# Performance work log

Measured on AMD Instinct MI355X. Metric: run time of the kernel, lower is better.

## Reference

```python
import jax, jax.numpy as jnp
import numpy as np

D_MODEL = 768
N_HEADS = 12
D_HEAD = D_MODEL // N_HEADS
TEMP = float(np.sqrt(D_HEAD))


def setup_inputs() -> dict:
    key = jax.random.key(0)
    ks = jax.random.split(key, 12)
    B, S, D = 8, 2048, D_MODEL
    patches = jax.random.normal(ks[0], (B, S, D), dtype=jnp.float32)
    in_weight = jax.random.uniform(ks[1], (D * 3, D), dtype=jnp.float32)
    in_bias = jax.random.uniform(ks[2], (D * 3,), dtype=jnp.float32)
    out_w = jax.random.normal(ks[3], (D, D), dtype=jnp.float32) * (1.0 / np.sqrt(D))
    out_b = jnp.zeros((D,), dtype=jnp.float32)
    mlp_w1 = jax.random.normal(ks[4], (4 * D, D), dtype=jnp.float32) * (1.0 / np.sqrt(D))
    mlp_b1 = jnp.zeros((4 * D,), dtype=jnp.float32)
    mlp_w2 = jax.random.normal(ks[5], (D, 4 * D), dtype=jnp.float32) * (1.0 / np.sqrt(4 * D))
    mlp_b2 = jnp.zeros((D,), dtype=jnp.float32)
    ln1_g = jnp.ones((D,), dtype=jnp.float32)
    ln1_b = jnp.zeros((D,), dtype=jnp.float32)
    ln2_g = jnp.ones((D,), dtype=jnp.float32)
    ln2_b = jnp.zeros((D,), dtype=jnp.float32)
    return {
        "patches": patches,
        "in_weight": in_weight, "in_bias": in_bias,
        "out_w": out_w, "out_b": out_b,
        "mlp_w1": mlp_w1, "mlp_b1": mlp_b1,
        "mlp_w2": mlp_w2, "mlp_b2": mlp_b2,
        "ln1_g": ln1_g, "ln1_b": ln1_b,
        "ln2_g": ln2_g, "ln2_b": ln2_b,
    }


def layer_norm(x, g, b, eps=1e-5):
    mu = jnp.mean(x, axis=-1, keepdims=True)
    var = jnp.var(x, axis=-1, keepdims=True)
    return (x - mu) * jax.lax.rsqrt(var + eps) * g + b


def mha(x, in_weight, in_bias, out_w, out_b):
    # Replicate quirky per-head reshape: [3D, D] -> [H, d_head, 3, D]
    W = in_weight.reshape(N_HEADS, D_HEAD, 3, D_MODEL)  # h, e, 3, d
    Bv = in_bias.reshape(N_HEADS, D_HEAD, 3)            # h, e, 3
    qw, kw, vw = W[:, :, 0, :], W[:, :, 1, :], W[:, :, 2, :]  # [H, e, D]
    qb, kb, vb = Bv[:, :, 0], Bv[:, :, 1], Bv[:, :, 2]        # [H, e]
    # Q,K,V per head: [B, H, S, e]
    Q = jnp.einsum('bsd,hed->bhse', x, qw) + qb[None, :, None, :]
    K = jnp.einsum('bsd,hed->bhse', x, kw) + kb[None, :, None, :]
    V = jnp.einsum('bsd,hed->bhse', x, vw) + vb[None, :, None, :]
    atn = jnp.einsum('bhse,bhte->bhst', Q, K)
    atn = jax.nn.softmax(atn / TEMP, axis=-1)
    # NOTE: original uses V (not atn @ V) as head output; heads concatenated over feature dim
    B_, H, S, e = V.shape
    heads = jnp.transpose(V, (0, 2, 1, 3)).reshape(B_, S, H * e)
    masks = jnp.sum(atn, axis=1)  # sum over heads: [B, S, S]
    out = heads @ out_w.T + out_b
    return out, masks


def reference(patches, in_weight, in_bias, out_w, out_b,
              mlp_w1, mlp_b1, mlp_w2, mlp_b2,
              ln1_g, ln1_b, ln2_g, ln2_b):
    x = layer_norm(patches, ln1_g, ln1_b)
    sa, _ = mha(x, in_weight, in_bias, out_w, out_b)
    x = sa + x  # dropout = identity (eval)
    x = layer_norm(x, ln2_g, ln2_b)
    h = jax.nn.selu(x @ mlp_w1.T + mlp_b1)
    x = (h @ mlp_w2.T + mlp_b2) + x
    return x
```

## Files before the change

kernel.cpp:

```cpp
#include <hip/hip_runtime.h>


typedef __bf16 bf16;
typedef __bf16 bf16x8 __attribute__((ext_vector_type(8)));
typedef __bf16 bf16x4 __attribute__((ext_vector_type(4)));
typedef float  f32x4  __attribute__((ext_vector_type(4)));

#define N_ROWS  16384

#define AS1(p) ((const __attribute__((address_space(1))) void*)(p))
#define AS3(p) ((__attribute__((address_space(3))) void*)(p))

#define WAIT8  __builtin_amdgcn_s_waitcnt(0x0F78)
#define WAIT6  __builtin_amdgcn_s_waitcnt(0x0F76)
#define WAIT2  __builtin_amdgcn_s_waitcnt(0x0F72)
#define WAIT0  __builtin_amdgcn_s_waitcnt(0x0F70)
#define NOWAIT (void)0

#define N1 589824
#define N2 589824
#define N3 147456
__global__ __launch_bounds__(256) void prep_cast(const float* __restrict__ w1,
                                                 const float* __restrict__ w2,
                                                 const float* __restrict__ ow,
                                                 bf16* __restrict__ w1b,
                                                 bf16* __restrict__ w2b,
                                                 bf16* __restrict__ owb) {
  int i = blockIdx.x * 256 + threadIdx.x;
  const float* src; bf16* dst; int off;
  if (i < N1)           { src = w1; dst = w1b; off = i; }
  else if (i < N1 + N2) { src = w2; dst = w2b; off = i - N1; }
  else                  { src = ow; dst = owb; off = i - N1 - N2; }
  float4 v = ((const float4*)src)[off];
  bf16x4 o = {(bf16)v.x, (bf16)v.y, (bf16)v.z, (bf16)v.w};
  *(bf16x4*)(dst + 4 * (size_t)off) = o;
}

__global__ __launch_bounds__(256) void wvt_kernel(const float* __restrict__ in_weight,
                                                  bf16* __restrict__ wvt) {
  __shared__ float t[64][65];
  const int k0 = blockIdx.x * 64, j0 = blockIdx.y * 64;
  const int tx = threadIdx.x & 63, ty = threadIdx.x >> 6;
  for (int jj = ty; jj < 64; jj += 4)
    t[jj][tx] = in_weight[((size_t)(j0 + jj) * 3 + 2) * 768 + k0 + tx];
  __syncthreads();
  for (int kk = ty; kk < 64; kk += 4)
    wvt[(size_t)(k0 + kk) * 768 + j0 + tx] = (bf16)t[tx][kk];
}

__global__ __launch_bounds__(64) void bias_combine_kernel(const float* __restrict__ out_w,
                                                          const float* __restrict__ in_bias,
                                                          const float* __restrict__ out_b,
                                                          float* __restrict__ bc) {
  int n = blockIdx.x, l = threadIdx.x;
  float s = 0.f;
  for (int j = l; j < 768; j += 64) s += out_w[(size_t)n * 768 + j] * in_bias[j * 3 + 2];
#pragma unroll
  for (int off = 32; off > 0; off >>= 1) s += __shfl_xor(s, off, 64);
  if (l == 0) bc[n] = s + out_b[n];
}

template <typename TIN>
__global__ __launch_bounds__(256) void ln_kernel(const TIN* __restrict__ x,
                                                 const float* __restrict__ g,
                                                 const float* __restrict__ b,
                                                 bf16* __restrict__ y) {
  const int row = blockIdx.x;
  const TIN* xr = x + (size_t)row * 768;
  float v[3], s1 = 0.f, s2 = 0.f;
#pragma unroll
  for (int i = 0; i < 3; ++i) {
    v[i] = (float)xr[threadIdx.x + i * 256];
    s1 += v[i];
    s2 += v[i] * v[i];
  }
#pragma unroll
  for (int off = 32; off > 0; off >>= 1) {
    s1 += __shfl_xor(s1, off, 64);
    s2 += __shfl_xor(s2, off, 64);
  }
  __shared__ float red[8];
  int w = threadIdx.x >> 6, l = threadIdx.x & 63;
  if (l == 0) { red[w * 2] = s1; red[w * 2 + 1] = s2; }
  __syncthreads();
  s1 = red[0] + red[2] + red[4] + red[6];
  s2 = red[1] + red[3] + red[5] + red[7];
  const float mu = s1 * (1.f / 768.f);
  const float var = s2 * (1.f / 768.f) - mu * mu;
  const float rstd = rsqrtf(var + 1e-5f);
#pragma unroll
  for (int i = 0; i < 3; ++i) {
    int d = threadIdx.x + i * 256;
    y[(size_t)row * 768 + d] = (bf16)((v[i] - mu) * rstd * g[d] + b[d]);
  }
}

template <int EPI>
__global__ __launch_bounds__(512, 2) void gemm_bt(const bf16* __restrict__ A,
                                                  const bf16* __restrict__ B,
                                                  const float* __restrict__ bias,
                                                  const bf16* __restrict__ resid,
                                                  void* __restrict__ out,
                                                  int M, int N, int K) {
  __shared__ bf16 ring[65536];
  const int tid = threadIdx.x;
  const int w = tid >> 6, l = tid & 63;
  const int wr = w >> 2, wcn = w & 3;
  const int q = l >> 4, m16 = l & 15;

  int mtile, ntile;
  {
    const int L = blockIdx.y * gridDim.x + blockIdx.x;
    const int gy = gridDim.y;
    if ((gy & 7) == 0) {
      const int mpx = gy >> 3;
      const int xcd = L & 7;
      const int slot = L >> 3;
      mtile = xcd * mpx + (slot % mpx);
      ntile = slot / mpx;
    } else {
      mtile = blockIdx.y; ntile = blockIdx.x;
    }
  }
  const long tileM = (long)mtile * 256;
  const long tileN = (long)ntile * 256;

  const bf16* gA[2][2]; const bf16* gB[2][2];
  int lA[2][2], lB[2][2];
  {
    const int sc = l & 3;
#pragma unroll
    for (int j = 0; j < 2; ++j) {
      const int b = w * 2 + j;
      const int p = b >> 3, s = (b >> 2) & 1, blk = b & 3;
#pragma unroll
      for (int mh = 0; mh < 2; ++mh) {
        const int row = s * 128 + mh * 64 + blk * 16 + (l >> 2);
        const int cl = (sc - (row >> 1)) & 3;
        gA[mh][j] = A + (tileM + row) * (long)K + p * 32 + cl * 8;
        lA[mh][j] = p * 8192 + row * 32 + sc * 8;
      }
      const int rowB = b * 16 + (l >> 2);
      const int clB = (sc - (rowB >> 1)) & 3;
#pragma unroll
      for (int ks = 0; ks < 2; ++ks) {
        gB[ks][j] = B + (tileN + rowB) * (long)K + ks * 32 + clB * 8;
        lB[ks][j] = 16384 + ks * 8192 + rowB * 32 + sc * 8;
      }
    }
  }

  int offA[8], offB[4];
#pragma unroll
  for (int mh = 0; mh < 2; ++mh)
#pragma unroll
    for (int mi = 0; mi < 4; ++mi) {
      const int r = wr * 128 + mh * 64 + mi * 16 + m16;
      offA[mh * 4 + mi] = r * 32 + (((q + (r >> 1)) & 3) << 3);
    }
#pragma unroll
  for (int ni = 0; ni < 4; ++ni) {
    const int r = wcn * 64 + ni * 16 + m16;
    offB[ni] = r * 32 + (((q + (r >> 1)) & 3) << 3);
  }

  f32x4 acc[8][4] = {};

  int kb0A0 = 0, kb0B0 = 0, kb0B1 = 0, kb0A1 = 0;
  int kb1A0 = 64, kb1B0 = 64, kb1B1 = 64, kb1A1 = 64;

#define ST(BP, LO, BUF, KV)                                                    \
  { bf16* bb = ring + (BUF) * 32768;                                           \
    __builtin_amdgcn_global_load_lds(AS1((BP)[0] + (KV)), AS3(bb + (LO)[0]), 16, 0, 0); \
    __builtin_amdgcn_global_load_lds(AS1((BP)[1] + (KV)), AS3(bb + (LO)[1]), 16, 0, 0); \
    (KV) += 128; }

  ST(gA[0], lA[0], 0, kb0A0) ST(gB[0], lB[0], 0, kb0B0)
  ST(gA[1], lA[1], 0, kb0A1) ST(gB[1], lB[1], 0, kb0B1)
  ST(gB[1], lB[1], 1, kb1B1) ST(gA[1], lA[1], 1, kb1A1)
  WAIT6;
  __builtin_amdgcn_s_barrier();

  bf16x8 bv[4];
#define PHASE(BUF, MH, KS, LB, STG, WSTMT)                                     \
  {                                                                            \
    const bf16* pa = ring + (BUF) * 32768 + (KS) * 8192;                       \
    const bf16* pb = ring + (BUF) * 32768 + 16384 + (KS) * 8192;               \
    bf16x8 af[4];                                                              \
    _Pragma("unroll")                                                          \
    for (int mi = 0; mi < 4; ++mi)                                             \
      af[mi] = *(const bf16x8*)&pa[offA[(MH) * 4 + mi]];                       \
    if (LB) {                                                                  \
      _Pragma("unroll")                                                        \
      for (int ni = 0; ni < 4; ++ni)                                           \
        bv[ni] = *(const bf16x8*)&pb[offB[ni]];                                \
    }                                                                          \
    STG;                                                                       \
    WSTMT;                                                                     \
    __builtin_amdgcn_s_barrier();                                              \
    asm volatile("s_waitcnt lgkmcnt(0)");                                      \
    __builtin_amdgcn_s_setprio(1);                                             \
    _Pragma("unroll")                                                          \
    for (int mi = 0; mi < 4; ++mi) {                                           \
      _Pragma("unroll")                                                        \
      for (int ni = 0; ni < 4; ++ni)                                           \
        acc[(MH) * 4 + mi][ni] = __builtin_amdgcn_mfma_f32_16x16x32_bf16(      \
            af[mi], bv[ni], acc[(MH) * 4 + mi][ni], 0, 0, 0);                  \
    }                                                                          \
    __builtin_amdgcn_s_setprio(0);                                             \
    __builtin_amdgcn_s_barrier();                                              \
  }

  const int T = K >> 6;
#pragma unroll 1
  for (int i = 0; i < T / 2 - 1; ++i) {
    PHASE(0, 0, 0, 1, ST(gA[0], lA[0], 1, kb1A0), NOWAIT)
    PHASE(0, 1, 0, 0, ST(gB[0], lB[0], 1, kb1B0), WAIT8)
    PHASE(0, 1, 1, 1, ST(gB[0], lB[0], 0, kb0B0), NOWAIT)
    PHASE(0, 0, 1, 0, ST(gA[1], lA[1], 0, kb0A1), WAIT6)
    PHASE(1, 0, 1, 1, ST(gA[0], lA[0], 0, kb0A0), NOWAIT)
    PHASE(1, 1, 1, 0, ST(gB[1], lB[1], 0, kb0B1), WAIT8)
    PHASE(1, 1, 0, 1, ST(gB[1], lB[1], 1, kb1B1), NOWAIT)
    PHASE(1, 0, 0, 0, ST(gA[1], lA[1], 1, kb1A1), WAIT6)
  }
  PHASE(0, 0, 0, 1, ST(gA[0], lA[0], 1, kb1A0), NOWAIT)
  PHASE(0, 1, 0, 0, ST(gB[0], lB[0], 1, kb1B0), WAIT8)
  PHASE(0, 1, 1, 1, (void)0, NOWAIT)
  PHASE(0, 0, 1, 0, (void)0, WAIT2)
  PHASE(1, 0, 1, 1, (void)0, NOWAIT)
  PHASE(1, 1, 1, 0, (void)0, WAIT0)
  PHASE(1, 1, 0, 1, (void)0, NOWAIT)
  PHASE(1, 0, 0, 0, (void)0, NOWAIT)
#undef PHASE
#undef ST

  const long colBase = tileN + (long)wcn * 64 + m16;
  const long rowBase = tileM + (long)wr * 128 + q * 4;
#pragma unroll
  for (int mi = 0; mi < 8; ++mi) {
#pragma unroll
    for (int r = 0; r < 4; ++r) {
      const long row = rowBase + mi * 16 + r;
#pragma unroll
      for (int ni = 0; ni < 4; ++ni) {
        const long col = colBase + ni * 16;
        float v = acc[mi][ni][r];
        if (EPI == 0) {
          ((bf16*)out)[row * N + col] = (bf16)v;
        } else if (EPI == 1) {
          v += bias[col] + (float)resid[row * N + col];
          ((float*)out)[row * N + col] = v;
        } else if (EPI == 2) {
          v += bias[col];
          v = v > 0.f ? 1.0507009873554805f * v
                      : 1.0507009873554805f * 1.6732632423543772f * (__expf(v) - 1.f);
          ((bf16*)out)[row * N + col] = (bf16)v;
        } else {
          v += bias[col] + (float)resid[row * N + col];
          ((bf16*)out)[row * N + col] = (bf16)v;
        }
      }
    }
  }
}

extern "C" void kernel_launch(void* const* d_in, const int* in_sizes, int n_in,
                              void* d_out, int out_size, void* d_ws, size_t ws_size,
                              hipStream_t stream) {
  const float* patches   = (const float*)d_in[0];
  const float* in_weight = (const float*)d_in[1];
  const float* in_bias   = (const float*)d_in[2];
  const float* out_w     = (const float*)d_in[3];
  const float* out_b     = (const float*)d_in[4];
  const float* mlp_w1    = (const float*)d_in[5];
  const float* mlp_b1    = (const float*)d_in[6];
  const float* mlp_w2    = (const float*)d_in[7];
  const float* mlp_b2    = (const float*)d_in[8];
  const float* ln1_g     = (const float*)d_in[9];
  const float* ln1_b     = (const float*)d_in[10];
  const float* ln2_g     = (const float*)d_in[11];
  const float* ln2_b     = (const float*)d_in[12];

  char* ws = (char*)d_ws;
  const size_t MB = 1024 * 1024;
  bf16* Wc   = (bf16*)(ws + 0);
  bf16* w1b  = (bf16*)(ws + 2 * MB);
  bf16* w2b  = (bf16*)(ws + 8 * MB);
  bf16* owb  = (bf16*)(ws + 14 * MB);
  bf16* wvt  = (bf16*)(ws + 16 * MB);
  float* bc  = (float*)(ws + 18 * MB);
  bf16* X1   = (bf16*)(ws + 20 * MB);
  bf16* X3   = (bf16*)(ws + 20 * MB);
  bf16* X2b  = (bf16*)(ws + 48 * MB);
  bf16* H    = (bf16*)(ws + 48 * MB);

  prep_cast<<<(N1 + N2 + N3) / 256, 256, 0, stream>>>(mlp_w1, mlp_w2, out_w,
                                                      w1b, w2b, owb);
  wvt_kernel<<<dim3(12, 12), 256, 0, stream>>>(in_weight, wvt);
  bias_combine_kernel<<<768, 64, 0, stream>>>(out_w, in_bias, out_b, bc);
  gemm_bt<0><<<dim3(3, 3), 512, 0, stream>>>(owb, wvt, nullptr, nullptr, Wc, 768, 768, 768);

  ln_kernel<float><<<N_ROWS, 256, 0, stream>>>(patches, ln1_g, ln1_b, X1);
  gemm_bt<3><<<dim3(3, 64), 512, 0, stream>>>(X1, Wc, bc, X1, X2b, N_ROWS, 768, 768);
  ln_kernel<bf16><<<N_ROWS, 256, 0, stream>>>(X2b, ln2_g, ln2_b, X3);
  gemm_bt<2><<<dim3(12, 64), 512, 0, stream>>>(X3, w1b, mlp_b1, nullptr, H, N_ROWS, 3072, 768);
  gemm_bt<1><<<dim3(3, 64), 512, 0, stream>>>(H, w2b, mlp_b2, X3, d_out, N_ROWS, 768, 3072);
}
```

Baseline: 390.1 us.

## Add 128x128-tile GEMM kernel with 3-stage LDS ring for MLP GEMMs

```diff
diff --git a/kernel.cpp b/kernel.cpp
--- a/kernel.cpp
+++ b/kernel.cpp
@@ -11,6 +11,8 @@
 #define AS1(p) ((const __attribute__((address_space(1))) void*)(p))
 #define AS3(p) ((__attribute__((address_space(3))) void*)(p))
 
+#define VM4 0x0F74
+#define VM0 0x0F70
 #define WAIT8  __builtin_amdgcn_s_waitcnt(0x0F78)
 #define WAIT6  __builtin_amdgcn_s_waitcnt(0x0F76)
 #define WAIT2  __builtin_amdgcn_s_waitcnt(0x0F72)
@@ -95,8 +97,145 @@
   }
 }
 
+#define SLOT_E (256 * 32)
 template <int EPI>
-__global__ __launch_bounds__(512, 2) void gemm_bt(const bf16* __restrict__ A,
+__global__ __launch_bounds__(256, 3) void gemm128(const bf16* __restrict__ A,
+                                                  const bf16* __restrict__ B,
+                                                  const float* __restrict__ bias,
+                                                  const bf16* __restrict__ resid,
+                                                  void* __restrict__ out,
+                                                  int M, int N, int K) {
+  __shared__ bf16 ring[3 * SLOT_E];
+  const int tid = threadIdx.x;
+  const int w = tid >> 6, l = tid & 63;
+  const int wr = w >> 1, wcn = w & 1;
+  const int q = l >> 4, m16 = l & 15;
+
+  int mtile, ntile;
+  {
+    const int L = blockIdx.y * gridDim.x + blockIdx.x;
+    const int gy = gridDim.y;
+    if ((gy & 7) == 0) {
+      const int mpx = gy >> 3;
+      const int xcd = L & 7;
+      const int slot = L >> 3;
+      mtile = xcd * mpx + (slot % mpx);
+      ntile = slot / mpx;
+    } else {
+      mtile = blockIdx.y; ntile = blockIdx.x;
+    }
+  }
+  const long tileM = (long)mtile * 128;
+  const long tileN = (long)ntile * 128;
+
+  const bf16* gA[2]; int ldA[2];
+  const bf16* gB[2]; int ldB[2];
+#pragma unroll
+  for (int j = 0; j < 2; ++j) {
+    const int ch = tid + j * 256;
+    const int row = ch >> 2;
+    const int cl = ((ch & 3) - (row >> 1)) & 3;
+    gA[j] = A + (tileM + row) * (long)K + cl * 8;
+    gB[j] = B + (tileN + row) * (long)K + cl * 8;
+    ldA[j] = ch * 8;
+    ldB[j] = ch * 8;
+  }
+
+  int offA[4], offB[4];
+#pragma unroll
+  for (int mi = 0; mi < 4; ++mi) {
+    const int r = wr * 64 + mi * 16 + m16;
+    offA[mi] = r * 32 + (((q + (r >> 1)) & 3) << 3);
+  }
+#pragma unroll
+  for (int ni = 0; ni < 4; ++ni) {
+    const int r = wcn * 64 + ni * 16 + m16;
+    offB[ni] = r * 32 + (((q + (r >> 1)) & 3) << 3);
+  }
+
+  f32x4 acc[4][4] = {};
+
+#pragma unroll
+  for (int s = 0; s < 2; ++s) {
+    bf16* da = ring + s * SLOT_E;
+    bf16* db = da + 128 * 32;
+#pragma unroll
+    for (int j = 0; j < 2; ++j) {
+      __builtin_amdgcn_global_load_lds(AS1(gA[j] + s * 32), AS3(&da[ldA[j]]), 16, 0, 0);
+      __builtin_amdgcn_global_load_lds(AS1(gB[j] + s * 32), AS3(&db[ldB[j]]), 16, 0, 0);
+    }
+  }
+  long k_next = 64;
+
+#define KSTEP(SLOT, WIMM, ISSUE)                                               \
+  {                                                                            \
+    __builtin_amdgcn_s_waitcnt(WIMM);                                          \
+    __builtin_amdgcn_s_barrier();                                              \
+    if (ISSUE) {                                                               \
+      bf16* da = ring + (((SLOT) + 2) % 3) * SLOT_E;                           \
+      bf16* db = da + 128 * 32;                                                \
+      _Pragma("unroll")                                                        \
+      for (int j = 0; j < 2; ++j) {                                            \
+        __builtin_amdgcn_global_load_lds(AS1(gA[j] + k_next), AS3(&da[ldA[j]]), 16, 0, 0); \
+        __builtin_amdgcn_global_load_lds(AS1(gB[j] + k_next), AS3(&db[ldB[j]]), 16, 0, 0); \
+      }                                                                        \
+      k_next += 32;                                                            \
+    }                                                                          \
+    const bf16* ca = ring + (SLOT) * SLOT_E;                                   \
+    const bf16* cb = ca + 128 * 32;                                            \
+    bf16x8 bfr[4];                                                             \
+    _Pragma("unroll")                                                          \
+    for (int ni = 0; ni < 4; ++ni) bfr[ni] = *(const bf16x8*)&cb[offB[ni]];    \
+    _Pragma("unroll")                                                          \
+    for (int mi = 0; mi < 4; ++mi) {                                           \
+      const bf16x8 af = *(const bf16x8*)&ca[offA[mi]];                         \
+      _Pragma("unroll")                                                        \
+      for (int ni = 0; ni < 4; ++ni)                                           \
+        acc[mi][ni] = __builtin_amdgcn_mfma_f32_16x16x32_bf16(af, bfr[ni],     \
+                                                              acc[mi][ni], 0, 0, 0); \
+    }                                                                          \
+  }
+
+  const int T = K >> 5;
+#pragma unroll 1
+  for (int g = 0; g < T - 3; g += 3) {
+    KSTEP(0, VM4, 1) KSTEP(1, VM4, 1) KSTEP(2, VM4, 1)
+  }
+  KSTEP(0, VM4, 1) KSTEP(1, VM4, 0) KSTEP(2, VM0, 0)
+#undef KSTEP
+
+  const long colBase = tileN + (long)wcn * 64 + m16;
+  const long rowBase = tileM + (long)wr * 64 + q * 4;
+#pragma unroll
+  for (int mi = 0; mi < 4; ++mi) {
+#pragma unroll
+    for (int r = 0; r < 4; ++r) {
+      const long row = rowBase + mi * 16 + r;
+#pragma unroll
+      for (int ni = 0; ni < 4; ++ni) {
+        const long col = colBase + ni * 16;
+        float v = acc[mi][ni][r];
+        if (EPI == 0) {
+          ((bf16*)out)[row * N + col] = (bf16)v;
+        } else if (EPI == 1) {
+          v += bias[col] + (float)resid[row * N + col];
+          ((float*)out)[row * N + col] = v;
+        } else if (EPI == 2) {
+          v += bias[col];
+          v = v > 0.f ? 1.0507009873554805f * v
+                      : 1.0507009873554805f * 1.6732632423543772f * (__expf(v) - 1.f);
+          ((bf16*)out)[row * N + col] = (bf16)v;
+        } else {
+          v += bias[col] + (float)resid[row * N + col];
+          ((bf16*)out)[row * N + col] = (bf16)v;
+        }
+      }
+    }
+  }
+}
+
+template <int EPI>
+__global__ __launch_bounds__(512, 2) void gemm256(const bf16* __restrict__ A,
                                                   const bf16* __restrict__ B,
                                                   const float* __restrict__ bias,
                                                   const bf16* __restrict__ resid,
@@ -298,11 +437,11 @@
                                                       w1b, w2b, owb);
   wvt_kernel<<<dim3(12, 12), 256, 0, stream>>>(in_weight, wvt);
   bias_combine_kernel<<<768, 64, 0, stream>>>(out_w, in_bias, out_b, bc);
-  gemm_bt<0><<<dim3(3, 3), 512, 0, stream>>>(owb, wvt, nullptr, nullptr, Wc, 768, 768, 768);
+  gemm256<0><<<dim3(3, 3), 512, 0, stream>>>(owb, wvt, nullptr, nullptr, Wc, 768, 768, 768);
 
   ln_kernel<float><<<N_ROWS, 256, 0, stream>>>(patches, ln1_g, ln1_b, X1);
-  gemm_bt<3><<<dim3(3, 64), 512, 0, stream>>>(X1, Wc, bc, X1, X2b, N_ROWS, 768, 768);
+  gemm256<3><<<dim3(3, 64), 512, 0, stream>>>(X1, Wc, bc, X1, X2b, N_ROWS, 768, 768);
   ln_kernel<bf16><<<N_ROWS, 256, 0, stream>>>(X2b, ln2_g, ln2_b, X3);
-  gemm_bt<2><<<dim3(12, 64), 512, 0, stream>>>(X3, w1b, mlp_b1, nullptr, H, N_ROWS, 3072, 768);
-  gemm_bt<1><<<dim3(3, 64), 512, 0, stream>>>(H, w2b, mlp_b2, X3, d_out, N_ROWS, 768, 3072);
-}
+  gemm128<2><<<dim3(24, 128), 256, 0, stream>>>(X3, w1b, mlp_b1, nullptr, H, N_ROWS, 3072, 768);
+  gemm128<1><<<dim3(6, 128), 256, 0, stream>>>(H, w2b, mlp_b2, X3, d_out, N_ROWS, 768, 3072);
+}
```

Result: slower. 412.7 us (+5.8%).
